# Kernel tuning notes

Hardware: AMD Instinct MI355X
Metric: run time of the kernel (lower is better)

Reference implementation:

```python
import jax, jax.numpy as jnp
import numpy as np

V, D, H, L, T_BLK = 32000, 1024, 16, 8, 512
HS = D // H
EPS = 1e-6
NEG_SLOPE = 0.1


def setup_inputs() -> dict:
    key = jax.random.key(0)
    ks = jax.random.split(key, 20)
    s = 0.02
    inp = {
        "idx": jax.random.randint(ks[0], (8, 512), 0, V),
        "tok_embed": jax.random.normal(ks[1], (V, D), jnp.float32) * s,
        "pos_embed": jax.random.normal(ks[2], (T_BLK, D), jnp.float32) * s,
        # per-layer stacked per-head QKV projections (bias=True)
        "Wq": jax.random.normal(ks[3], (L, H, D, HS), jnp.float32) * s,
        "bq": jnp.zeros((L, H, HS), jnp.float32),
        "Wk": jax.random.normal(ks[4], (L, H, D, HS), jnp.float32) * s,
        "bk": jnp.zeros((L, H, HS), jnp.float32),
        "Wv": jax.random.normal(ks[5], (L, H, D, HS), jnp.float32) * s,
        "bv": jnp.zeros((L, H, HS), jnp.float32),
        "Wo": jax.random.normal(ks[6], (L, D, D), jnp.float32) * s,
        "bo": jnp.zeros((L, D), jnp.float32),
        "W1": jax.random.normal(ks[7], (L, D, 4 * D), jnp.float32) * s,
        "b1": jnp.zeros((L, 4 * D), jnp.float32),
        "W2": jax.random.normal(ks[8], (L, 4 * D, D), jnp.float32) * s,
        "b2": jnp.zeros((L, D), jnp.float32),
        "norm_w": jnp.ones((L, D), jnp.float32),
        "final_norm_w": jnp.ones((D,), jnp.float32),
        "Wf": jax.random.normal(ks[9], (D, V), jnp.float32) * s,
        "bf": jnp.zeros((V,), jnp.float32),
    }
    return inp


def _rmsnorm(x, w):
    return x * jax.lax.rsqrt(jnp.mean(x * x, axis=-1, keepdims=True) + EPS) * w


def _attn(x, Wq, bq, Wk, bk, Wv, bv, Wo, bo, masked):
    B, T, _ = x.shape
    q = jnp.einsum('btd,hde->bhte', x, Wq) + bq[:, None, :]
    k = jnp.einsum('btd,hde->bhte', x, Wk) + bk[:, None, :]
    v = jnp.einsum('btd,hde->bhte', x, Wv) + bv[:, None, :]
    # faithful to source: scores / hs**(-0.5) == scores * sqrt(hs)
    scores = jnp.einsum('bhte,bhse->bhts', q, k) * (HS ** 0.5)
    if masked:
        causal = jnp.tril(jnp.ones((T, T), bool))
        scores = jnp.where(causal, scores, -jnp.inf)
    att = jax.nn.softmax(scores, axis=-1)
    out = jnp.einsum('bhts,bhse->bthe', att, v).reshape(B, T, D)
    return out @ Wo + bo


def _ffn(x, W1, b1, W2, b2):
    h = x @ W1 + b1
    h = jnp.where(h >= 0, h, NEG_SLOPE * h)
    return h @ W2 + b2


def reference(idx, tok_embed, pos_embed, Wq, bq, Wk, bk, Wv, bv, Wo, bo,
              W1, b1, W2, b2, norm_w, final_norm_w, Wf, bf):
    B, T = idx.shape
    x = tok_embed[idx] + pos_embed[jnp.arange(T)]
    for l in range(L):
        nw = norm_w[l]
        # unmasked self-attention (shared weights with masked call below)
        x_out = x + _attn(_rmsnorm(x, nw), Wq[l], bq[l], Wk[l], bk[l],
                          Wv[l], bv[l], Wo[l], bo[l], masked=False)
        # FFN, residual from ORIGINAL x (faithful to source)
        x_out = x + _ffn(_rmsnorm(x_out, nw), W1[l], b1[l], W2[l], b2[l])
        # masked self-attention with the SAME attention weights
        x = x_out + _attn(_rmsnorm(x_out, nw), Wq[l], bq[l], Wk[l], bk[l],
                          Wv[l], bv[l], Wo[l], bo[l], masked=True)
    logits = _rmsnorm(x, final_norm_w) @ Wf + bf
    return logits
```

## Files before the change

### kernel.cpp

```cpp
#include <hip/hip_runtime.h>
#include <hip/hip_bf16.h>
#include <cstdint>
#include <cstddef>

#define T_SEQ   512
#define BATCH   8
#define BT      4096
#define DMODEL  1024
#define NHEAD   16
#define HSZ     64
#define NLAYER  8
#define DFF     4096
#define VOCAB   32000
#define EPS     1e-6f
#define NEG_SLOPE 0.1f
#define QLD     3072
#define MSCALE  2048.0f
#define MINV    (1.0f / 2048.0f)

typedef _Float16 f16;
typedef __attribute__((ext_vector_type(8))) _Float16 half8;
typedef __attribute__((ext_vector_type(4))) _Float16 half4;
typedef __attribute__((ext_vector_type(4))) float f32x4;

#define AS1 __attribute__((address_space(1)))
#define AS3 __attribute__((address_space(3)))

#define WAIT_BAR(N) asm volatile("s_waitcnt vmcnt(" #N ")\ns_barrier" ::: "memory")
#define LGKM_BAR()  asm volatile("s_waitcnt lgkmcnt(0)\ns_barrier" ::: "memory")

__global__ void embed_kernel(const int* __restrict__ idx,
                             const float* __restrict__ tok,
                             const float* __restrict__ pos,
                             float* __restrict__ x) {
    int bt  = blockIdx.x;
    int tid = threadIdx.x;
    int token = idx[bt];
    int t = bt & (T_SEQ - 1);
    float4 a = reinterpret_cast<const float4*>(tok + (size_t)token * DMODEL)[tid];
    float4 p = reinterpret_cast<const float4*>(pos + (size_t)t * DMODEL)[tid];
    reinterpret_cast<float4*>(x + (size_t)bt * DMODEL)[tid] =
        make_float4(a.x + p.x, a.y + p.y, a.z + p.z, a.w + p.w);
}

__device__ __forceinline__ void split2h(float v, f16& h, f16& m) {
    f16 hh = (f16)v;
    float hf = (float)hh;
    if (fabsf(hf) < 6.103515625e-05f) { hh = (f16)0.0f; hf = 0.0f; }
    h = hh;
    m = (f16)((v - hf) * MSCALE);
}

__global__ void rms_split(const float* __restrict__ x,
                          const float* __restrict__ w,
                          f16* __restrict__ out, size_t planeStride) {
    int row = blockIdx.x;
    int tid = threadIdx.x;
    float4 v = reinterpret_cast<const float4*>(x + (size_t)row * DMODEL)[tid];
    float ss = v.x * v.x + v.y * v.y + v.z * v.z + v.w * v.w;
#pragma unroll
    for (int off = 32; off > 0; off >>= 1) ss += __shfl_xor(ss, off);
    __shared__ float wsum[4];
    if ((tid & 63) == 0) wsum[tid >> 6] = ss;
    __syncthreads();
    float tot = wsum[0] + wsum[1] + wsum[2] + wsum[3];
    float scale = rsqrtf(tot * (1.0f / DMODEL) + EPS);
    float4 wv = reinterpret_cast<const float4*>(w)[tid];
    float o[4] = {v.x * scale * wv.x, v.y * scale * wv.y,
                  v.z * scale * wv.z, v.w * scale * wv.w};
    size_t base = (size_t)row * DMODEL + tid * 4;
#pragma unroll
    for (int j = 0; j < 4; ++j) {
        f16 h, m;
        split2h(o[j], h, m);
        out[base + j] = h;
        out[planeStride + base + j] = m;
    }
}

__global__ __launch_bounds__(256)
void transpose_split(const float* __restrict__ in, f16* __restrict__ out,
                     size_t planeStride, int R, int C,
                     long izs, long ozi) {
    int z = blockIdx.z;
    in  += (size_t)z * izs;
    out += (size_t)z * ozi;
    __shared__ float tile[32][33];
    int r0 = blockIdx.y << 5, c0 = blockIdx.x << 5;
    int tx = threadIdx.x & 31, ty = threadIdx.x >> 5;
#pragma unroll
    for (int i = 0; i < 4; ++i) {
        int r = ty + (i << 3);
        tile[r][tx] = in[(size_t)(r0 + r) * C + c0 + tx];
    }
    __syncthreads();
#pragma unroll
    for (int i = 0; i < 4; ++i) {
        int c = ty + (i << 3);
        float v = tile[tx][c];
        size_t o = (size_t)(c0 + c) * R + r0 + tx;
        f16 h, m;
        split2h(v, h, m);
        out[o] = h;
        out[planeStride + o] = m;
    }
}

__global__ void cat_bias(const float* __restrict__ bq, const float* __restrict__ bk,
                         const float* __restrict__ bv, float* __restrict__ cb) {
    int i = blockIdx.x * 256 + threadIdx.x;
    int l = i / QLD, r = i - l * QLD;
    const float* src = (r < 1024) ? bq : ((r < 2048) ? bk : bv);
    cb[i] = src[l * 1024 + (r & 1023)];
}

template <bool LRELU, bool SPLITOUT, bool VOUT>
__global__ __launch_bounds__(512, 4)
void gemm_f16(const f16* __restrict__ A, size_t aPS,
              const f16* __restrict__ Bt, size_t bPS,
              const float* __restrict__ bias,
              const float* __restrict__ resid,
              float* __restrict__ C, f16* __restrict__ Cp, size_t cPS,
              f16* __restrict__ vTp, size_t vPS,
              int N, int K) {
    __shared__ f16 As[2][2 * 4096];
    __shared__ f16 Bs[2][2 * 4096];

    int chunk = gridDim.x >> 3;
    int bid = blockIdx.x;
    int sw = (bid & 7) * chunk + (bid >> 3);
    int m0 = (sw & 31) << 7;
    int n0 = (sw >> 5) << 7;

    const int tid  = threadIdx.x;
    const int lane = tid & 63;
    const int wid  = tid >> 6;

    const int ssk = (((tid & 3) ^ ((tid >> 3) & 3)) << 3);
    const size_t offA = (size_t)(m0 + (tid >> 2)) * K + ssk;
    const size_t offB = (size_t)(n0 + (tid >> 2)) * K + ssk;
    const int ldst = wid * 512;

    f32x4 accH[4][2], accM[4][2];
#pragma unroll
    for (int i = 0; i < 4; ++i)
#pragma unroll
        for (int j = 0; j < 2; ++j) {
            accH[i][j] = (f32x4){0.f, 0.f, 0.f, 0.f};
            accM[i][j] = (f32x4){0.f, 0.f, 0.f, 0.f};
        }

    const int wr = wid >> 2, wc = wid & 3;
    const int fm = lane & 15;
    const int rslot = (((lane >> 4) ^ ((lane >> 1) & 3)) & 3) << 3;
    const int foffA0 = (wr * 64 + fm) * 32 + rslot;
    const int foffB0 = (wc * 32 + fm) * 32 + rslot;

    auto STAGE = [&](int buf, int k0) {
#pragma unroll
        for (int pp = 0; pp < 2; ++pp)
            __builtin_amdgcn_global_load_lds(
                (const AS1 void*)(A + pp * aPS + offA + k0),
                (AS3 void*)(&As[buf][pp * 4096 + ldst]), 16, 0, 0);
#pragma unroll
        for (int pp = 0; pp < 2; ++pp)
            __builtin_amdgcn_global_load_lds(
                (const AS1 void*)(Bt + pp * bPS + offB + k0),
                (AS3 void*)(&Bs[buf][pp * 4096 + ldst]), 16, 0, 0);
    };

    const int nt = K >> 5;
    STAGE(0, 0);
    int cur = 0;
    for (int t = 0; t < nt; ++t) {
        if (t + 1 < nt) {
            STAGE(cur ^ 1, (t + 1) << 5);
            WAIT_BAR(4);
        } else {
            WAIT_BAR(0);
        }

        half8 bh[2], bm[2];
#pragma unroll
        for (int j = 0; j < 2; ++j) {
            bh[j] = *(const half8*)(&Bs[cur][foffB0 + j * 512]);
            bm[j] = *(const half8*)(&Bs[cur][4096 + foffB0 + j * 512]);
        }
#pragma unroll
        for (int i = 0; i < 4; ++i) {
            half8 ah = *(const half8*)(&As[cur][foffA0 + i * 512]);
            half8 am = *(const half8*)(&As[cur][4096 + foffA0 + i * 512]);
#pragma unroll
            for (int j = 0; j < 2; ++j) {
                accM[i][j] = __builtin_amdgcn_mfma_f32_16x16x32_f16(
                    am, bh[j], accM[i][j], 0, 0, 0);
                accM[i][j] = __builtin_amdgcn_mfma_f32_16x16x32_f16(
                    ah, bm[j], accM[i][j], 0, 0, 0);
                accH[i][j] = __builtin_amdgcn_mfma_f32_16x16x32_f16(
                    ah, bh[j], accH[i][j], 0, 0, 0);
            }
        }
        LGKM_BAR();
        cur ^= 1;
    }

    const bool vblock = VOUT && (n0 >= 2048);
#pragma unroll
    for (int i = 0; i < 4; ++i) {
        int mbase = m0 + wr * 64 + i * 16 + ((lane >> 4) << 2);
#pragma unroll
        for (int j = 0; j < 2; ++j) {
            int n = n0 + wc * 32 + j * 16 + fm;
            float bv = bias[n];
            if (vblock) {
                half4 ph4, pm4;
#pragma unroll
                for (int rr = 0; rr < 4; ++rr) {
                    float v = accH[i][j][rr] + accM[i][j][rr] * MINV + bv;
                    f16 hh, mm;
                    split2h(v, hh, mm);
                    ph4[rr] = hh;
                    pm4[rr] = mm;
                }
                int nn = n - 2048;
                int bb = mbase >> 9, tt = mbase & 511;
                size_t vo = (((size_t)(bb * 16 + (nn >> 6)) * 64 + (nn & 63)) << 9) + tt;
                *(half4*)(vTp + vo) = ph4;
                *(half4*)(vTp + vPS + vo) = pm4;
            } else {
#pragma unroll
                for (int rr = 0; rr < 4; ++rr) {
                    int m = mbase + rr;
                    float v = accH[i][j][rr] + accM[i][j][rr] * MINV + bv;
                    if (LRELU) v = (v >= 0.f) ? v : NEG_SLOPE * v;
                    size_t o = (size_t)m * N + n;
                    if (SPLITOUT) {
                        f16 h, mm;
                        split2h(v, h, mm);
                        Cp[o] = h;
                        Cp[cPS + o] = mm;
                    } else {
                        if (resid) v += resid[o];
                        C[o] = v;
                    }
                }
            }
        }
    }
}

__global__ __launch_bounds__(512, 4)
void gemm_f16_1p(const f16* __restrict__ A,
                 const f16* __restrict__ Bt,
                 const float* __restrict__ bias,
                 float* __restrict__ C, int N, int K) {
    __shared__ f16 As[2][4096];
    __shared__ f16 Bs[2][4096];

    int chunk = gridDim.x >> 3;
    int bid = blockIdx.x;
    int sw = (bid & 7) * chunk + (bid >> 3);
    int m0 = (sw & 31) << 7;
    int n0 = (sw >> 5) << 7;

    const int tid  = threadIdx.x;
    const int lane = tid & 63;
    const int wid  = tid >> 6;

    const int ssk = (((tid & 3) ^ ((tid >> 3) & 3)) << 3);
    const size_t offA = (size_t)(m0 + (tid >> 2)) * K + ssk;
    const size_t offB = (size_t)(n0 + (tid >> 2)) * K + ssk;
    const int ldst = wid * 512;

    f32x4 acc[4][2];
#pragma unroll
    for (int i = 0; i < 4; ++i)
#pragma unroll
        for (int j = 0; j < 2; ++j) acc[i][j] = (f32x4){0.f, 0.f, 0.f, 0.f};

    const int wr = wid >> 2, wc = wid & 3;
    const int fm = lane & 15;
    const int rslot = (((lane >> 4) ^ ((lane >> 1) & 3)) & 3) << 3;
    const int foffA0 = (wr * 64 + fm) * 32 + rslot;
    const int foffB0 = (wc * 32 + fm) * 32 + rslot;

    auto STAGE = [&](int buf, int k0) {
        __builtin_amdgcn_global_load_lds((const AS1 void*)(A + offA + k0),
                                         (AS3 void*)(&As[buf][ldst]), 16, 0, 0);
        __builtin_amdgcn_global_load_lds((const AS1 void*)(Bt + offB + k0),
                                         (AS3 void*)(&Bs[buf][ldst]), 16, 0, 0);
    };

    const int nt = K >> 5;
    STAGE(0, 0);
    int cur = 0;
    for (int t = 0; t < nt; ++t) {
        if (t + 1 < nt) {
            STAGE(cur ^ 1, (t + 1) << 5);
            WAIT_BAR(2);
        } else {
            WAIT_BAR(0);
        }

        half8 bh[2];
#pragma unroll
        for (int j = 0; j < 2; ++j)
            bh[j] = *(const half8*)(&Bs[cur][foffB0 + j * 512]);
#pragma unroll
        for (int i = 0; i < 4; ++i) {
            half8 ah = *(const half8*)(&As[cur][foffA0 + i * 512]);
#pragma unroll
            for (int j = 0; j < 2; ++j)
                acc[i][j] = __builtin_amdgcn_mfma_f32_16x16x32_f16(
                    ah, bh[j], acc[i][j], 0, 0, 0);
        }
        LGKM_BAR();
        cur ^= 1;
    }

#pragma unroll
    for (int i = 0; i < 4; ++i) {
        int mbase = m0 + wr * 64 + i * 16 + ((lane >> 4) << 2);
#pragma unroll
        for (int j = 0; j < 2; ++j) {
            int n = n0 + wc * 32 + j * 16 + fm;
            float bv = bias[n];
#pragma unroll
            for (int rr = 0; rr < 4; ++rr) {
                int m = mbase + rr;
                __builtin_nontemporal_store(acc[i][j][rr] + bv,
                                            C + (size_t)m * N + n);
            }
        }
    }
}

template <int CAUSAL>
__global__ __launch_bounds__(256)
void attn_mfma(const f16* __restrict__ qkvp, size_t QPS,
               const f16* __restrict__ vT, size_t VPS,
               f16* __restrict__ outp, size_t OPS) {
    __shared__ f16 lds[24576];
    const int tid  = threadIdx.x;
    const int lane = tid & 63;
    const int wid  = tid >> 6;
    const int tl   = lane & 15;
    const int g    = lane >> 4;

    int bh = blockIdx.y;
    int b = bh >> 4, h = bh & 15;
    int t0 = blockIdx.x << 6;
    const int PB = 16384 + wid * 2048;

    half8 Qh[2], Qm[2];
    {
        const f16* qb = qkvp + (size_t)(b * 512 + t0 + wid * 16 + tl) * 3072
                        + h * 64 + (g << 3);
        Qh[0] = *(const half8*)(qb);
        Qh[1] = *(const half8*)(qb + 32);
        Qm[0] = *(const half8*)(qb + QPS);
        Qm[1] = *(const half8*)(qb + QPS + 32);
    }

    f32x4 oH[4], oM[4];
#pragma unroll
    for (int en = 0; en < 4; ++en) {
        oH[en] = (f32x4){0.f, 0.f, 0.f, 0.f};
        oM[en] = (f32x4){0.f, 0.f, 0.f, 0.f};
    }
    float m_run = -INFINITY, l_run = 0.f;

    auto STAGE1 = [&](int ldsOff, const f16* srcBase, int rowStride) {
#pragma unroll
        for (int it = 0; it < 2; ++it) {
            int r  = (tid >> 3) + it * 32;
            int cp = (tid & 7) ^ (r & 7);
            __builtin_amdgcn_global_load_lds(
                (const AS1 void*)(srcBase + (size_t)r * rowStride + cp * 8),
                (AS3 void*)(lds + ldsOff + (it * 32 + wid * 8) * 64), 16, 0, 0);
        }
    };

    const int NT = CAUSAL ? (blockIdx.x + 1) : (T_SEQ / 64);
    for (int st = 0; st < NT; ++st) {
        int s0 = st << 6;
        {
            const f16* kS = qkvp + (size_t)(b * 512 + s0) * 3072 + 1024 + h * 64;
            const f16* vS = vT + ((size_t)(bh * 64) << 9) + s0;
            STAGE1(0,     kS, 3072);
            STAGE1(4096,  kS + QPS, 3072);
            STAGE1(8192,  vS, 512);
            STAGE1(12288, vS + VPS, 512);
        }
        __syncthreads();

        f32x4 sH[4], sM[4];
#pragma unroll
        for (int sm = 0; sm < 4; ++sm) {
            sH[sm] = (f32x4){0.f, 0.f, 0.f, 0.f};
            sM[sm] = (f32x4){0.f, 0.f, 0.f, 0.f};
        }
#pragma unroll
        for (int sm = 0; sm < 4; ++sm) {
            int sl = sm * 16 + tl;
#pragma unroll
            for (int kf = 0; kf < 2; ++kf) {
                int sp = ((kf * 4 + g) ^ (sl & 7)) << 3;
                half8 kh = *(const half8*)(lds + sl * 64 + sp);
                half8 km = *(const half8*)(lds + 4096 + sl * 64 + sp);
                sM[sm] = __builtin_amdgcn_mfma_f32_16x16x32_f16(km, Qh[kf], sM[sm], 0, 0, 0);
                sM[sm] = __builtin_amdgcn_mfma_f32_16x16x32_f16(kh, Qm[kf], sM[sm], 0, 0, 0);
                sH[sm] = __builtin_amdgcn_mfma_f32_16x16x32_f16(kh, Qh[kf], sH[sm], 0, 0, 0);
            }
        }

        float sv[4][4];
#pragma unroll
        for (int sm = 0; sm < 4; ++sm)
#pragma unroll
            for (int rr = 0; rr < 4; ++rr) {
                float v = (sH[sm][rr] + sM[sm][rr] * MINV) * 8.0f;
                if (CAUSAL && st == NT - 1) {
                    int sg = s0 + sm * 16 + (g << 2) + rr;
                    int tg = t0 + wid * 16 + tl;
                    if (sg > tg) v = -INFINITY;
                }
                sv[sm][rr] = v;
            }
        float rmax = -INFINITY;
#pragma unroll
        for (int sm = 0; sm < 4; ++sm)
#pragma unroll
            for (int rr = 0; rr < 4; ++rr) rmax = fmaxf(rmax, sv[sm][rr]);
        rmax = fmaxf(rmax, __shfl_xor(rmax, 16));
        rmax = fmaxf(rmax, __shfl_xor(rmax, 32));
        float mn = fmaxf(m_run, rmax);
        float fsc = __expf(m_run - mn);
        float rs = 0.f;
#pragma unroll
        for (int sm = 0; sm < 4; ++sm)
#pragma unroll
            for (int rr = 0; rr < 4; ++rr) {
                float p = __expf(sv[sm][rr] - mn);
                sv[sm][rr] = p;
                rs += p;
            }
        rs += __shfl_xor(rs, 16);
        rs += __shfl_xor(rs, 32);
        l_run = l_run * fsc + rs;
        m_run = mn;
#pragma unroll
        for (int en = 0; en < 4; ++en)
#pragma unroll
            for (int rr = 0; rr < 4; ++rr) {
                oH[en][rr] *= fsc;
                oM[en][rr] *= fsc;
            }

#pragma unroll
        for (int sm = 0; sm < 4; ++sm) {
            half4 ph4, pm4;
#pragma unroll
            for (int rr = 0; rr < 4; ++rr) {
                f16 hh, mm;
                split2h(sv[sm][rr], hh, mm);
                ph4[rr] = hh;
                pm4[rr] = mm;
            }
            int sbase = sm * 16 + (g << 2);
            int sp = (sbase >> 3) ^ (tl & 7);
            int eo = PB + tl * 64 + sp * 8 + (sbase & 7);
            *(half4*)(lds + eo) = ph4;
            *(half4*)(lds + eo + 1024) = pm4;
        }
        asm volatile("s_waitcnt lgkmcnt(0)" ::: "memory");
        __builtin_amdgcn_sched_barrier(0);

        half8 Ph[2], Pm[2];
#pragma unroll
        for (int kf = 0; kf < 2; ++kf) {
            int sp = ((kf * 4 + g) ^ (tl & 7)) << 3;
            Ph[kf] = *(const half8*)(lds + PB + tl * 64 + sp);
            Pm[kf] = *(const half8*)(lds + PB + 1024 + tl * 64 + sp);
        }
#pragma unroll
        for (int en = 0; en < 4; ++en) {
            int el = en * 16 + tl;
#pragma unroll
            for (int kf = 0; kf < 2; ++kf) {
                int sp = ((kf * 4 + g) ^ (el & 7)) << 3;
                half8 vh = *(const half8*)(lds + 8192 + el * 64 + sp);
                half8 vm = *(const half8*)(lds + 12288 + el * 64 + sp);
                oM[en] = __builtin_amdgcn_mfma_f32_16x16x32_f16(vm, Ph[kf], oM[en], 0, 0, 0);
                oM[en] = __builtin_amdgcn_mfma_f32_16x16x32_f16(vh, Pm[kf], oM[en], 0, 0, 0);
                oH[en] = __builtin_amdgcn_mfma_f32_16x16x32_f16(vh, Ph[kf], oH[en], 0, 0, 0);
            }
        }
        __syncthreads();
    }

    float inv = 1.f / l_run;
    size_t obase = (size_t)(b * 512 + t0 + wid * 16 + tl) * 1024 + h * 64;
#pragma unroll
    for (int en = 0; en < 4; ++en) {
        half4 ph4, pm4;
#pragma unroll
        for (int rr = 0; rr < 4; ++rr) {
            float v = (oH[en][rr] + oM[en][rr] * MINV) * inv;
            f16 hh, mm;
            split2h(v, hh, mm);
            ph4[rr] = hh;
            pm4[rr] = mm;
        }
        size_t oc = obase + en * 16 + (g << 2);
        *(half4*)(outp + oc) = ph4;
        *(half4*)(outp + OPS + oc) = pm4;
    }
}

extern "C" void kernel_launch(void* const* d_in, const int* in_sizes, int n_in,
                              void* d_out, int out_size, void* d_ws, size_t ws_size,
                              hipStream_t stream) {
    const int*   idx = (const int*)  d_in[0];
    const float* tok = (const float*)d_in[1];
    const float* pos = (const float*)d_in[2];
    const float* Wq  = (const float*)d_in[3];
    const float* bq  = (const float*)d_in[4];
    const float* Wk  = (const float*)d_in[5];
    const float* bk  = (const float*)d_in[6];
    const float* Wv  = (const float*)d_in[7];
    const float* bv  = (const float*)d_in[8];
    const float* Wo  = (const float*)d_in[9];
    const float* bo  = (const float*)d_in[10];
    const float* W1  = (const float*)d_in[11];
    const float* b1  = (const float*)d_in[12];
    const float* W2  = (const float*)d_in[13];
    const float* b2  = (const float*)d_in[14];
    const float* nw  = (const float*)d_in[15];
    const float* fnw = (const float*)d_in[16];
    const float* Wf  = (const float*)d_in[17];
    const float* bf  = (const float*)d_in[18];
    float* out = (float*)d_out;

    const size_t SZ   = (size_t)BT * DMODEL;
    const size_t HSZF = (size_t)BT * DFF;
    const size_t QPS  = (size_t)BT * QLD;
    const size_t VPS  = (size_t)BATCH * NHEAD * HSZ * T_SEQ;

    char* w = (char*)d_ws;
    auto alloc = [&](size_t bytes) {
        char* p = w;
        w += (bytes + 255) & ~(size_t)255;
        return p;
    };
    float* x    = (float*)alloc(SZ * 4);
    float* xo   = (float*)alloc(SZ * 4);
    f16*   xnp  = (f16*)  alloc(SZ * 2 * 2);
    f16*   qkvp = (f16*)  alloc(QPS * 2 * 2);
    f16*   vTb  = (f16*)  alloc(VPS * 2 * 2);
    f16*   aop  = (f16*)  alloc(SZ * 2 * 2);
    f16*   hbp  = (f16*)  alloc(HSZF * 2 * 2);
    char*  wreg = alloc(132ull * 1024 * 1024);
    f16*   qkvTp = (f16*)wreg;
    f16*   woTp  = qkvTp + 2ull * QLD * DMODEL;
    f16*   w1Tp  = woTp  + 2ull * DMODEL * DMODEL;
    f16*   w2Tp  = w1Tp  + 2ull * DFF * DMODEL;
    f16*   wfp   = (f16*)wreg;
    float* catb  = (float*)alloc((size_t)NLAYER * QLD * 4);

    cat_bias<<<(NLAYER * QLD) / 256, 256, 0, stream>>>(bq, bk, bv, catb);
    embed_kernel<<<BT, 256, 0, stream>>>(idx, tok, pos, x);

    for (int l = 0; l < NLAYER; ++l) {
        const float* nwl = nw + (size_t)l * DMODEL;
        const float* catbl = catb + (size_t)l * QLD;
        const float* bol = bo + (size_t)l * DMODEL;
        const float* b1l = b1 + (size_t)l * DFF;
        const float* b2l = b2 + (size_t)l * DMODEL;

        {
            long izs = (long)DMODEL * HSZ;
            long ozi = (long)HSZ * DMODEL;
            size_t ps = (size_t)QLD * DMODEL;
            dim3 gq(HSZ / 32, DMODEL / 32, NHEAD);
            const float* Wql = Wq + (size_t)l * NHEAD * DMODEL * HSZ;
            const float* Wkl = Wk + (size_t)l * NHEAD * DMODEL * HSZ;
            const float* Wvl = Wv + (size_t)l * NHEAD * DMODEL * HSZ;
            transpose_split<<<gq, 256, 0, stream>>>(Wql, qkvTp,                 ps, DMODEL, HSZ, izs, ozi);
            transpose_split<<<gq, 256, 0, stream>>>(Wkl, qkvTp + 1024ul * 1024, ps, DMODEL, HSZ, izs, ozi);
            transpose_split<<<gq, 256, 0, stream>>>(Wvl, qkvTp + 2048ul * 1024, ps, DMODEL, HSZ, izs, ozi);
            transpose_split<<<dim3(DMODEL / 32, DMODEL / 32, 1), 256, 0, stream>>>(
                Wo + (size_t)l * DMODEL * DMODEL, woTp, (size_t)DMODEL * DMODEL, DMODEL, DMODEL, 0, 0);
            transpose_split<<<dim3(DFF / 32, DMODEL / 32, 1), 256, 0, stream>>>(
                W1 + (size_t)l * DMODEL * DFF, w1Tp, (size_t)DFF * DMODEL, DMODEL, DFF, 0, 0);
            transpose_split<<<dim3(DMODEL / 32, DFF / 32, 1), 256, 0, stream>>>(
                W2 + (size_t)l * DMODEL * DFF, w2Tp, (size_t)DMODEL * DFF, DFF, DMODEL, 0, 0);
        }

        auto attn = [&](const float* resid, float* outp, int causal) {
            gemm_f16<false, true, true><<<dim3((BT / 128) * (QLD / 128)), 512, 0, stream>>>(
                xnp, SZ, qkvTp, (size_t)QLD * DMODEL, catbl, nullptr,
                nullptr, qkvp, QPS, vTb, VPS, QLD, DMODEL);
            if (causal)
                attn_mfma<1><<<dim3(T_SEQ / 64, BATCH * NHEAD), 256, 0, stream>>>(
                    qkvp, QPS, vTb, VPS, aop, SZ);
            else
                attn_mfma<0><<<dim3(T_SEQ / 64, BATCH * NHEAD), 256, 0, stream>>>(
                    qkvp, QPS, vTb, VPS, aop, SZ);
            gemm_f16<false, false, false><<<dim3((BT / 128) * (DMODEL / 128)), 512, 0, stream>>>(
                aop, SZ, woTp, (size_t)DMODEL * DMODEL, bol, resid,
                outp, nullptr, 0, nullptr, 0, DMODEL, DMODEL);
        };

        rms_split<<<BT, 256, 0, stream>>>(x, nwl, xnp, SZ);
        attn(x, xo, 0);
        rms_split<<<BT, 256, 0, stream>>>(xo, nwl, xnp, SZ);
        gemm_f16<true, true, false><<<dim3((BT / 128) * (DFF / 128)), 512, 0, stream>>>(
            xnp, SZ, w1Tp, (size_t)DFF * DMODEL, b1l, nullptr,
            nullptr, hbp, HSZF, nullptr, 0, DFF, DMODEL);
        gemm_f16<false, false, false><<<dim3((BT / 128) * (DMODEL / 128)), 512, 0, stream>>>(
            hbp, HSZF, w2Tp, (size_t)DMODEL * DFF, b2l, x,
            xo, nullptr, 0, nullptr, 0, DMODEL, DFF);
        rms_split<<<BT, 256, 0, stream>>>(xo, nwl, xnp, SZ);
        attn(xo, x, 1);
    }

    rms_split<<<BT, 256, 0, stream>>>(x, fnw, xnp, SZ);
    transpose_split<<<dim3(VOCAB / 32, DMODEL / 32, 1), 256, 0, stream>>>(
        Wf, wfp, (size_t)VOCAB * DMODEL, DMODEL, VOCAB, 0, 0);
    gemm_f16_1p<<<dim3((BT / 128) * (VOCAB / 128)), 512, 0, stream>>>(
        xnp, wfp, bf, out, VOCAB, DMODEL);
}
```

Baseline: 6.356 ms.

## Single-buffer B tile in GEMM and swizzle attention block order across XCDs

The GEMM now keeps only one LDS buffer for the B tile and double-buffers A. After B fragments are read into registers and an LDS wait completes, the next B tile is issued mid-iteration, before the MFMA work. This cuts LDS use and may raise occupancy, but it shortens how far the B load is hidden and adds an extra wait per iteration. The attention kernel moves to a 1D grid whose index is remapped so that blocks for the same batch-head fall in the same XCD group, aiming for better L2 reuse of K/V.

```diff
diff --git a/kernel.cpp b/kernel.cpp
--- a/kernel.cpp
+++ b/kernel.cpp
@@ -124,7 +124,7 @@
               f16* __restrict__ vTp, size_t vPS,
               int N, int K) {
     __shared__ f16 As[2][2 * 4096];
-    __shared__ f16 Bs[2][2 * 4096];
+    __shared__ f16 Bs[2 * 4096];
 
     int chunk = gridDim.x >> 3;
     int bid = blockIdx.x;
@@ -156,26 +156,29 @@
     const int foffA0 = (wr * 64 + fm) * 32 + rslot;
     const int foffB0 = (wc * 32 + fm) * 32 + rslot;
 
-    auto STAGE = [&](int buf, int k0) {
+    auto STAGE_A = [&](int buf, int k0) {
 #pragma unroll
         for (int pp = 0; pp < 2; ++pp)
             __builtin_amdgcn_global_load_lds(
                 (const AS1 void*)(A + pp * aPS + offA + k0),
                 (AS3 void*)(&As[buf][pp * 4096 + ldst]), 16, 0, 0);
+    };
+    auto STAGE_B = [&](int k0) {
 #pragma unroll
         for (int pp = 0; pp < 2; ++pp)
             __builtin_amdgcn_global_load_lds(
                 (const AS1 void*)(Bt + pp * bPS + offB + k0),
-                (AS3 void*)(&Bs[buf][pp * 4096 + ldst]), 16, 0, 0);
+                (AS3 void*)(&Bs[pp * 4096 + ldst]), 16, 0, 0);
     };
 
     const int nt = K >> 5;
-    STAGE(0, 0);
+    STAGE_A(0, 0);
+    STAGE_B(0);
     int cur = 0;
     for (int t = 0; t < nt; ++t) {
         if (t + 1 < nt) {
-            STAGE(cur ^ 1, (t + 1) << 5);
-            WAIT_BAR(4);
+            STAGE_A(cur ^ 1, (t + 1) << 5);
+            WAIT_BAR(2);
         } else {
             WAIT_BAR(0);
         }
@@ -183,9 +186,12 @@
         half8 bh[2], bm[2];
 #pragma unroll
         for (int j = 0; j < 2; ++j) {
-            bh[j] = *(const half8*)(&Bs[cur][foffB0 + j * 512]);
-            bm[j] = *(const half8*)(&Bs[cur][4096 + foffB0 + j * 512]);
-        }
+            bh[j] = *(const half8*)(&Bs[foffB0 + j * 512]);
+            bm[j] = *(const half8*)(&Bs[4096 + foffB0 + j * 512]);
+        }
+        LGKM_BAR();
+        if (t + 1 < nt) STAGE_B((t + 1) << 5);
+
 #pragma unroll
         for (int i = 0; i < 4; ++i) {
             half8 ah = *(const half8*)(&As[cur][foffA0 + i * 512]);
@@ -347,9 +353,12 @@
     const int tl   = lane & 15;
     const int g    = lane >> 4;
 
-    int bh = blockIdx.y;
+    int bid = blockIdx.x;
+    int sw = ((bid & 7) << 7) + (bid >> 3);
+    int bh = sw >> 3;
+    int qt = sw & 7;
     int b = bh >> 4, h = bh & 15;
-    int t0 = blockIdx.x << 6;
+    int t0 = qt << 6;
     const int PB = 16384 + wid * 2048;
 
     half8 Qh[2], Qm[2];
@@ -381,7 +390,7 @@
         }
     };
 
-    const int NT = CAUSAL ? (blockIdx.x + 1) : (T_SEQ / 64);
+    const int NT = CAUSAL ? (qt + 1) : (T_SEQ / 64);
     for (int st = 0; st < NT; ++st) {
         int s0 = st << 6;
         {
@@ -602,10 +611,10 @@
                 xnp, SZ, qkvTp, (size_t)QLD * DMODEL, catbl, nullptr,
                 nullptr, qkvp, QPS, vTb, VPS, QLD, DMODEL);
             if (causal)
-                attn_mfma<1><<<dim3(T_SEQ / 64, BATCH * NHEAD), 256, 0, stream>>>(
+                attn_mfma<1><<<dim3(1024), 256, 0, stream>>>(
                     qkvp, QPS, vTb, VPS, aop, SZ);
             else
-                attn_mfma<0><<<dim3(T_SEQ / 64, BATCH * NHEAD), 256, 0, stream>>>(
+                attn_mfma<0><<<dim3(1024), 256, 0, stream>>>(
                     qkvp, QPS, vTb, VPS, aop, SZ);
             gemm_f16<false, false, false><<<dim3((BT / 128) * (DMODEL / 128)), 512, 0, stream>>>(
                 aop, SZ, woTp, (size_t)DMODEL * DMODEL, bol, resid,
```

New measurement: 5.980 ms. 1.06x faster.
